# Kernel tuning notes

Measured on AMD Instinct MI355X. Metric: run time of the kernel, lower is better.

## Reference

```python
import jax, jax.numpy as jnp
import numpy as np

SAMPLE_SIZE = 8192
K = 8
N_SPLATS = 1_000_000
EPS = 1e-12  # keeps sqrt grad finite on zero-distance (duplicate) pairs


def setup_inputs() -> dict:
    key = jax.random.key(0)
    k1, k2, k3 = jax.random.split(key, 3)
    means = jax.random.normal(k1, (N_SPLATS, 3), dtype=jnp.float32)
    sh0 = jax.random.normal(k2, (N_SPLATS, 1, 3), dtype=jnp.float32)
    idx = jax.random.randint(k3, (SAMPLE_SIZE,), 0, N_SPLATS, dtype=jnp.int64)
    return {"means": means, "sh0": sh0, "idx": idx}


def reference(means, sh0, idx):
    sh0 = sh0.squeeze(1)                    # [N, 3]
    sm = means[idx]                         # [S, 3] sampled positions
    ss = sh0[idx]                           # [S, 3] sampled colors
    # pairwise euclidean distances (torch.cdist, p=2): [S, S]
    sq = jnp.sum(sm * sm, axis=-1)
    d2 = sq[:, None] + sq[None, :] - 2.0 * (sm @ sm.T)
    dist = jnp.sqrt(jnp.maximum(d2, EPS))
    # k+1 smallest per row; drop self (column 0)
    _, knn_idx = jax.lax.top_k(-dist, K + 1)           # [S, K+1]
    knn_idx = knn_idx[:, 1:]                           # [S, K]
    neighbors_sh0 = ss[knn_idx]                        # [S, K, 3]
    neighbor_dist = jnp.take_along_axis(dist, knn_idx, axis=1)[..., None]  # [S, K, 1]
    weight = jnp.exp(-neighbor_dist)
    diff = ss[:, None, :] - neighbors_sh0              # [S, K, 3]
    return jnp.mean(weight * diff * diff)
```

## Files before the change

### kernel.cpp

```cpp
#include <hip/hip_runtime.h>
#include <float.h>
#include <math.h>

#define NSAMPLE 8192
#define KSEL 9
#define KNN 8
#define BLK 512
#define EPS_F 1e-12f

#define ROWS_PB 8
#define NBLOCKS (NSAMPLE / ROWS_PB)
#define RPT 8
#define LANES 64
#define KQT 16
#define BNDI 8
#define BATCH 4
#define SLOTS 256
#define SLOTP 257
#define BP 257
#define IDX_MASK 0x1FFFu
#define VAL_MASK 0xFFFFE000u
#define PROW 73
#define SROW 289
#define SCALE (1.0f / (float)(NSAMPLE * KNN * 3))

__device__ __forceinline__ unsigned umn(unsigned a, unsigned b) { return a < b ? a : b; }
__device__ __forceinline__ unsigned umx(unsigned a, unsigned b) { return a > b ? a : b; }

__device__ __forceinline__ void insert9(unsigned s[KSEL], unsigned x)
{
#pragma unroll
    for (int k = 0; k < KSEL - 1; ++k)
        s[k] = umx(s[k + 1], umn(x, s[k]));
    s[KSEL - 1] = umn(x, s[KSEL - 1]);
}

__device__ __forceinline__ unsigned pack_d2(float d2, int gidx)
{
    return (__float_as_uint(fmaxf(d2, 0.0f)) & VAL_MASK) | (unsigned)gidx;
}

__global__ __launch_bounds__(256) void gather_k(
    const float* __restrict__ means, const float* __restrict__ sh0,
    const int* __restrict__ idx,
    float4* __restrict__ sm4, float4* __restrict__ ss4)
{
    int i = blockIdx.x * 256 + threadIdx.x;
    if (i >= NSAMPLE) return;
    int id = idx[i];
    const float* m = means + 3 * id;
    const float* s = sh0 + 3 * id;
    float mx = m[0], my = m[1], mz = m[2];
    sm4[i] = make_float4(mx, my, mz, fmaf(mx, mx, fmaf(my, my, mz * mz)));
    ss4[i] = make_float4(s[0], s[1], s[2], 0.0f);
}

__global__ __launch_bounds__(BLK, 8) void main_k(
    const float4* __restrict__ sm4, const float4* __restrict__ ss4,
    float* __restrict__ partial)
{
    __shared__ unsigned surv[ROWS_PB * SLOTP];
    __shared__ unsigned scratch[ROWS_PB * SROW];
    __shared__ unsigned bpart[ROWS_PB * BP];
    __shared__ unsigned partS[ROWS_PB * PROW];
    __shared__ unsigned scnt[ROWS_PB];
    __shared__ unsigned bnd[ROWS_PB];
    __shared__ float    red[ROWS_PB];

    const int t = threadIdx.x;
    const int lane = t & (LANES - 1);
    const int w = t >> 6;
    if (t < ROWS_PB) scnt[t] = 0u;

    float cX[RPT], cY[RPT], cZ[RPT], cW[RPT];
#pragma unroll
    for (int i = 0; i < RPT; ++i) {
        float4 p = sm4[blockIdx.x * ROWS_PB + i];
        cX[i] = -2.0f * p.x; cY[i] = -2.0f * p.y; cZ[i] = -2.0f * p.z;
        cW[i] = p.w;
    }

    if (w < 4) {
        unsigned pm[RPT];
#pragma unroll
        for (int i = 0; i < RPT; ++i) pm[i] = 0xFFFFFFFFu;
        const int b0 = w * (BNDI * LANES);
#pragma unroll
        for (int k = 0; k < BNDI; ++k) {
            const int ci = b0 + k * LANES + lane;
            float4 q = sm4[ci];
#pragma unroll
            for (int i = 0; i < RPT; ++i) {
                float d2 = fmaf(cX[i], q.x,
                           fmaf(cY[i], q.y, fmaf(cZ[i], q.z, cW[i] + q.w)));
                pm[i] = umn(pm[i], pack_d2(d2, ci));
            }
        }
#pragma unroll
        for (int i = 0; i < RPT; ++i)
            bpart[i * BP + w * LANES + lane] = pm[i];
    }
    __syncthreads();

    if (t < 256) {
        const int r1 = t & (ROWS_PB - 1);
        const int g = t >> 3;
        unsigned s[KSEL];
#pragma unroll
        for (int k = 0; k < KSEL; ++k) s[k] = 0xFFFFFFFFu;
#pragma unroll
        for (int e = 0; e < 8; ++e)
            insert9(s, bpart[r1 * BP + g * 8 + e]);
#pragma unroll
        for (int k = 0; k < KSEL; ++k)
            scratch[r1 * SROW + g * KSEL + k] = s[k];
    }
    __syncthreads();
    if (t < 64) {
        const int r1 = t & (ROWS_PB - 1);
        const int mg = t >> 3;
        unsigned m[KSEL];
#pragma unroll
        for (int k = 0; k < KSEL; ++k) m[k] = 0xFFFFFFFFu;
#pragma unroll
        for (int e = 0; e < 4 * KSEL; ++e)
            insert9(m, scratch[r1 * SROW + (4 * mg) * KSEL + e]);
#pragma unroll
        for (int k = 0; k < KSEL; ++k)
            partS[r1 * PROW + mg * KSEL + k] = m[k];
    }
    __syncthreads();
    if (t < ROWS_PB) {
        unsigned m[KSEL];
#pragma unroll
        for (int k = 0; k < KSEL; ++k) m[k] = 0xFFFFFFFFu;
#pragma unroll
        for (int e = 0; e < 8 * KSEL; ++e)
            insert9(m, partS[t * PROW + e]);
        bnd[t] = m[0];
    }
    __syncthreads();

    float bf[RPT];
#pragma unroll
    for (int i = 0; i < RPT; ++i)
        bf[i] = __uint_as_float(bnd[i] | IDX_MASK);

    const int s0 = w * (KQT * LANES);
    for (int k0 = 0; k0 < KQT; k0 += BATCH) {
        float4 qr[BATCH];
#pragma unroll
        for (int u = 0; u < BATCH; ++u)
            qr[u] = sm4[s0 + (k0 + u) * LANES + lane];
#pragma unroll
        for (int u = 0; u < BATCH; ++u) {
            const int ci = s0 + (k0 + u) * LANES + lane;
#pragma unroll
            for (int i = 0; i < RPT; ++i) {
                float d2 = fmaf(cX[i], qr[u].x,
                           fmaf(cY[i], qr[u].y,
                           fmaf(cZ[i], qr[u].z, cW[i] + qr[u].w)));
                bool c = (d2 <= bf[i]);
                if (__any(c)) {
                    if (c) {
                        unsigned pos = atomicAdd(&scnt[i], 1u);
                        if (pos < SLOTS)
                            surv[i * SLOTP + pos] = pack_d2(d2, ci);
                    }
                }
            }
        }
    }
    __syncthreads();

    if (t < 256) {
        const int r1 = t & (ROWS_PB - 1);
        const int g = t >> 3;
        const unsigned n = umn(scnt[r1], SLOTS);
        unsigned s[KSEL];
#pragma unroll
        for (int k = 0; k < KSEL; ++k) s[k] = 0xFFFFFFFFu;
        for (unsigned k = g; k < n; k += 32)
            insert9(s, surv[r1 * SLOTP + k]);
#pragma unroll
        for (int k = 0; k < KSEL; ++k)
            scratch[r1 * SROW + g * KSEL + k] = s[k];
    }
    __syncthreads();
    if (t < 64) {
        const int r1 = t & (ROWS_PB - 1);
        const int mg = t >> 3;
        unsigned m[KSEL];
#pragma unroll
        for (int k = 0; k < KSEL; ++k) m[k] = 0xFFFFFFFFu;
#pragma unroll
        for (int e = 0; e < 4 * KSEL; ++e)
            insert9(m, scratch[r1 * SROW + (4 * mg) * KSEL + e]);
#pragma unroll
        for (int k = 0; k < KSEL; ++k)
            partS[r1 * PROW + mg * KSEL + k] = m[k];
    }
    __syncthreads();

    if (t < ROWS_PB) {
        unsigned m[KSEL];
#pragma unroll
        for (int k = 0; k < KSEL; ++k) m[k] = 0xFFFFFFFFu;
#pragma unroll
        for (int e = 0; e < 8 * KSEL; ++e)
            insert9(m, partS[t * PROW + e]);

        const int gr = blockIdx.x * ROWS_PB + t;
        float4 pm4 = sm4[gr];
        float4 ps4 = ss4[gr];
        float acc = 0.0f;
#pragma unroll
        for (int k = 0; k < KNN; ++k) {
            int j = (int)(m[k] & IDX_MASK);
            float4 qm = sm4[j];
            float dx = pm4.x - qm.x, dy = pm4.y - qm.y, dz = pm4.z - qm.z;
            float d2 = fmaf(dx, dx, fmaf(dy, dy, dz * dz));
            float d = sqrtf(fmaxf(d2, EPS_F));
            float wgt = expf(-d);
            float4 qs = ss4[j];
            float ax = ps4.x - qs.x, ay = ps4.y - qs.y, az = ps4.z - qs.z;
            acc += wgt * (ax * ax + ay * ay + az * az);
        }
        red[t] = acc;
    }
    __syncthreads();
    if (t == 0) {
        float ssum = 0.0f;
#pragma unroll
        for (int i = 0; i < ROWS_PB; ++i) ssum += red[i];
        partial[blockIdx.x] = ssum;
    }
}

__global__ __launch_bounds__(256) void reduce_k(
    const float* __restrict__ partial, float* __restrict__ out)
{
    __shared__ float sbuf[4];
    int t = threadIdx.x;
    float v = 0.0f;
    for (int i = t; i < NBLOCKS; i += 256) v += partial[i];
    for (int off = 32; off > 0; off >>= 1) v += __shfl_down(v, off);
    if ((t & 63) == 0) sbuf[t >> 6] = v;
    __syncthreads();
    if (t == 0) {
        float s = sbuf[0] + sbuf[1] + sbuf[2] + sbuf[3];
        out[0] = s * SCALE;
    }
}

extern "C" void kernel_launch(void* const* d_in, const int* in_sizes, int n_in,
                              void* d_out, int out_size, void* d_ws, size_t ws_size,
                              hipStream_t stream)
{
    const float* means = (const float*)d_in[0];
    const float* sh0   = (const float*)d_in[1];
    const int*   idxp  = (const int*)d_in[2];

    float4* sm4 = (float4*)d_ws;
    float4* ss4 = sm4 + NSAMPLE;
    float*  partial = (float*)(ss4 + NSAMPLE);

    gather_k<<<NSAMPLE / 256, 256, 0, stream>>>(means, sh0, idxp, sm4, ss4);
    main_k<<<NBLOCKS, BLK, 0, stream>>>(sm4, ss4, partial);
    reduce_k<<<1, 256, 0, stream>>>(partial, (float*)d_out);
}
```

Before: 105.2 us.

## Split rows across wave pairs and use per-wave ballot-compacted survivor lists

Each wave now handles 4 of the 8 rows (split by row parity) over a quarter of the candidates, instead of all 8 rows over an eighth. Shared-memory atomicAdd survivor appends are replaced with ballot plus popcount compaction into per-wave, per-row lists capped at 32 entries, with a single any-check across the rows. The survivor merge shrinks to one pass over 32 lists followed by the final thread-per-row merge. This removes LDS atomic contention and one merge stage, at the risk of silently dropping candidates if a wave's list for a row exceeds 32 entries.

```diff
diff --git a/kernel.cpp b/kernel.cpp
--- a/kernel.cpp
+++ b/kernel.cpp
@@ -10,13 +10,12 @@
 
 #define ROWS_PB 8
 #define NBLOCKS (NSAMPLE / ROWS_PB)
-#define RPT 8
+#define RPT 4
 #define LANES 64
-#define KQT 16
+#define KQT 32
 #define BNDI 8
 #define BATCH 4
-#define SLOTS 256
-#define SLOTP 257
+#define WCAP 32
 #define BP 257
 #define IDX_MASK 0x1FFFu
 #define VAL_MASK 0xFFFFE000u
@@ -59,32 +58,34 @@
     const float4* __restrict__ sm4, const float4* __restrict__ ss4,
     float* __restrict__ partial)
 {
-    __shared__ unsigned surv[ROWS_PB * SLOTP];
+    __shared__ unsigned wl[8 * RPT * WCAP];
+    __shared__ unsigned wcnt[8 * RPT];
     __shared__ unsigned scratch[ROWS_PB * SROW];
     __shared__ unsigned bpart[ROWS_PB * BP];
     __shared__ unsigned partS[ROWS_PB * PROW];
-    __shared__ unsigned scnt[ROWS_PB];
     __shared__ unsigned bnd[ROWS_PB];
     __shared__ float    red[ROWS_PB];
 
     const int t = threadIdx.x;
     const int lane = t & (LANES - 1);
     const int w = t >> 6;
-    if (t < ROWS_PB) scnt[t] = 0u;
+    const int rpar = w & 1;
+    const int quarter = w >> 1;
+    const unsigned long long lmask_lt = (1ull << lane) - 1ull;
 
     float cX[RPT], cY[RPT], cZ[RPT], cW[RPT];
 #pragma unroll
     for (int i = 0; i < RPT; ++i) {
-        float4 p = sm4[blockIdx.x * ROWS_PB + i];
+        float4 p = sm4[blockIdx.x * ROWS_PB + rpar + 2 * i];
         cX[i] = -2.0f * p.x; cY[i] = -2.0f * p.y; cZ[i] = -2.0f * p.z;
         cW[i] = p.w;
     }
 
-    if (w < 4) {
+    {
         unsigned pm[RPT];
 #pragma unroll
         for (int i = 0; i < RPT; ++i) pm[i] = 0xFFFFFFFFu;
-        const int b0 = w * (BNDI * LANES);
+        const int b0 = quarter * (BNDI * LANES);
 #pragma unroll
         for (int k = 0; k < BNDI; ++k) {
             const int ci = b0 + k * LANES + lane;
@@ -98,7 +99,7 @@
         }
 #pragma unroll
         for (int i = 0; i < RPT; ++i)
-            bpart[i * BP + w * LANES + lane] = pm[i];
+            bpart[(rpar + 2 * i) * BP + quarter * LANES + lane] = pm[i];
     }
     __syncthreads();
 
@@ -144,9 +145,13 @@
     float bf[RPT];
 #pragma unroll
     for (int i = 0; i < RPT; ++i)
-        bf[i] = __uint_as_float(bnd[i] | IDX_MASK);
-
-    const int s0 = w * (KQT * LANES);
+        bf[i] = __uint_as_float(bnd[rpar + 2 * i] | IDX_MASK);
+
+    unsigned base[RPT];
+#pragma unroll
+    for (int i = 0; i < RPT; ++i) base[i] = 0u;
+
+    const int s0 = quarter * (KQT * LANES);
     for (int k0 = 0; k0 < KQT; k0 += BATCH) {
         float4 qr[BATCH];
 #pragma unroll
@@ -155,50 +160,53 @@
 #pragma unroll
         for (int u = 0; u < BATCH; ++u) {
             const int ci = s0 + (k0 + u) * LANES + lane;
-#pragma unroll
-            for (int i = 0; i < RPT; ++i) {
-                float d2 = fmaf(cX[i], qr[u].x,
-                           fmaf(cY[i], qr[u].y,
-                           fmaf(cZ[i], qr[u].z, cW[i] + qr[u].w)));
-                bool c = (d2 <= bf[i]);
-                if (__any(c)) {
-                    if (c) {
-                        unsigned pos = atomicAdd(&scnt[i], 1u);
-                        if (pos < SLOTS)
-                            surv[i * SLOTP + pos] = pack_d2(d2, ci);
+            float d2[RPT];
+#pragma unroll
+            for (int i = 0; i < RPT; ++i)
+                d2[i] = fmaf(cX[i], qr[u].x,
+                        fmaf(cY[i], qr[u].y,
+                        fmaf(cZ[i], qr[u].z, cW[i] + qr[u].w)));
+            float mrg = d2[0] - bf[0];
+#pragma unroll
+            for (int i = 1; i < RPT; ++i)
+                mrg = fminf(mrg, d2[i] - bf[i]);
+            if (__any(mrg <= 0.0f)) {
+#pragma unroll
+                for (int i = 0; i < RPT; ++i) {
+                    bool c = (d2[i] <= bf[i]);
+                    unsigned long long mk = __ballot(c);
+                    if (mk) {
+                        unsigned pos = base[i] +
+                            (unsigned)__popcll(mk & lmask_lt);
+                        if (c && pos < WCAP)
+                            wl[(w * RPT + i) * WCAP + pos] = pack_d2(d2[i], ci);
+                        base[i] += (unsigned)__popcll(mk);
                     }
                 }
             }
         }
     }
-    __syncthreads();
-
-    if (t < 256) {
+    if (lane == 0) {
+#pragma unroll
+        for (int i = 0; i < RPT; ++i)
+            wcnt[w * RPT + i] = umn(base[i], WCAP);
+    }
+    __syncthreads();
+
+    if (t < 32) {
         const int r1 = t & (ROWS_PB - 1);
-        const int g = t >> 3;
-        const unsigned n = umn(scnt[r1], SLOTS);
+        const int q = t >> 3;
+        const int wv = 2 * q + (r1 & 1);
+        const int li = wv * RPT + (r1 >> 1);
+        const unsigned n = wcnt[li];
         unsigned s[KSEL];
 #pragma unroll
         for (int k = 0; k < KSEL; ++k) s[k] = 0xFFFFFFFFu;
-        for (unsigned k = g; k < n; k += 32)
-            insert9(s, surv[r1 * SLOTP + k]);
+        for (unsigned k = 0; k < n; ++k)
+            insert9(s, wl[li * WCAP + k]);
 #pragma unroll
         for (int k = 0; k < KSEL; ++k)
-            scratch[r1 * SROW + g * KSEL + k] = s[k];
-    }
-    __syncthreads();
-    if (t < 64) {
-        const int r1 = t & (ROWS_PB - 1);
-        const int mg = t >> 3;
-        unsigned m[KSEL];
-#pragma unroll
-        for (int k = 0; k < KSEL; ++k) m[k] = 0xFFFFFFFFu;
-#pragma unroll
-        for (int e = 0; e < 4 * KSEL; ++e)
-            insert9(m, scratch[r1 * SROW + (4 * mg) * KSEL + e]);
-#pragma unroll
-        for (int k = 0; k < KSEL; ++k)
-            partS[r1 * PROW + mg * KSEL + k] = m[k];
+            partS[r1 * PROW + q * KSEL + k] = s[k];
     }
     __syncthreads();
 
@@ -207,7 +215,7 @@
 #pragma unroll
         for (int k = 0; k < KSEL; ++k) m[k] = 0xFFFFFFFFu;
 #pragma unroll
-        for (int e = 0; e < 8 * KSEL; ++e)
+        for (int e = 0; e < 4 * KSEL; ++e)
             insert9(m, partS[t * PROW + e]);
 
         const int gr = blockIdx.x * ROWS_PB + t;
```

New measurement: 101.5 us. 3.5% less time.
